# Optimization experiments

Measured on AMD Instinct MI355X. Metric: run time of the kernel, lower is better.

The kernel has to match this reference:

```python
import jax, jax.numpy as jnp
import numpy as np

B, S, T = 32, 50, 50
V_SRC, V_TRG = 32000, 32000
E, H, A = 128, 128, 128


def setup_inputs() -> dict:
    key = jax.random.key(0)
    ks = jax.random.split(key, 24)
    g = lambda k, shape, s=0.08: jax.random.normal(k, shape, dtype=jnp.float32) * s
    inp = {
        'src': jax.random.randint(ks[0], (B, S), 0, V_SRC, dtype=jnp.int32),
        'trg': jax.random.randint(ks[1], (B, T), 0, V_TRG, dtype=jnp.int32),
        'emb_src': g(ks[2], (V_SRC, E)),
        'emb_trg': g(ks[3], (V_TRG, E)),
        # PyTorch LSTM params: gates ordered (i, f, g, o)
        'enc_Wih': g(ks[4], (4 * H, E)), 'enc_Whh': g(ks[5], (4 * H, H)),
        'enc_bih': g(ks[6], (4 * H,)), 'enc_bhh': g(ks[7], (4 * H,)),
        'dec_Wih': g(ks[8], (4 * H, E)), 'dec_Whh': g(ks[9], (4 * H, H)),
        'dec_bih': g(ks[10], (4 * H,)), 'dec_bhh': g(ks[11], (4 * H,)),
        'att_w1s': g(ks[12], (A, H)), 'att_b1s': g(ks[13], (A,)),
        'att_w1t': g(ks[14], (A, H)), 'att_b1t': g(ks[15], (A,)),
        'att_w2': g(ks[16], (1, A)), 'att_b2': g(ks[17], (1,)),
        'out_w': g(ks[18], (H, 2 * H)), 'out_b': g(ks[19], (H,)),
        'sm_w': g(ks[20], (V_TRG, H)), 'sm_b': g(ks[21], (V_TRG,)),
    }
    return inp


def _lstm_cell(x, h, c, Wih, Whh, bih, bhh):
    gates = x @ Wih.T + bih + h @ Whh.T + bhh  # [B, 4H]
    i, f, g, o = jnp.split(gates, 4, axis=-1)
    c_new = jax.nn.sigmoid(f) * c + jax.nn.sigmoid(i) * jnp.tanh(g)
    h_new = jax.nn.sigmoid(o) * jnp.tanh(c_new)
    return h_new, c_new


def reference(src, trg, emb_src, emb_trg,
              enc_Wih, enc_Whh, enc_bih, enc_bhh,
              dec_Wih, dec_Whh, dec_bih, dec_bhh,
              att_w1s, att_b1s, att_w1t, att_b1t, att_w2, att_b2,
              out_w, out_b, sm_w, sm_b):
    batch = src.shape[0]
    hidden = enc_Whh.shape[1]
    h0 = jnp.zeros((batch, hidden), dtype=emb_src.dtype)
    c0 = jnp.zeros((batch, hidden), dtype=emb_src.dtype)

    # ---- encoder LSTM over src ----
    x_src = emb_src[src]                      # [B,S,E]
    def enc_step(carry, x_t):
        h, c = carry
        h, c = _lstm_cell(x_t, h, c, enc_Wih, enc_Whh, enc_bih, enc_bhh)
        return (h, c), h
    _, enc_out = jax.lax.scan(enc_step, (h0, c0), x_src.transpose(1, 0, 2))
    enc_out = enc_out.transpose(1, 0, 2)      # [B,S,H]

    # att_w1_src(src_vectors) is constant across decode steps
    att_src = enc_out @ att_w1s.T + att_b1s   # [B,S,A]

    # ---- decoder (init_hidden = zeros, per original forward) ----
    x_trg = emb_trg[trg[:, :-1]]              # [B,T-1,E]
    def dec_step(carry, x_t):
        h, c = carry
        h, c = _lstm_cell(x_t, h, c, dec_Wih, dec_Whh, dec_bih, dec_bhh)
        att_tgt = h @ att_w1t.T + att_b1t                       # [B,A]
        comb = jnp.tanh(att_src + att_tgt[:, None, :])          # [B,S,A]
        scores = (comb @ att_w2.T + att_b2)[..., 0]             # [B,S]
        align = jax.nn.softmax(scores, axis=1)
        att_vec = jnp.einsum('bs,bsh->bh', align, enc_out)      # [B,H]
        final = jnp.tanh(jnp.concatenate([h, att_vec], axis=1) @ out_w.T + out_b)
        logits = final @ sm_w.T + sm_b                          # [B,V]
        return (h, c), logits
    _, logits = jax.lax.scan(dec_step, (h0, c0), x_trg.transpose(1, 0, 2))
    return logits.transpose(1, 0, 2)          # [B,T-1,V]
```

## Files before the change

kernel.cpp:

```cpp
#include <hip/hip_runtime.h>

typedef unsigned short ushort_t;

__device__ __forceinline__ float sigf(float x) { return 1.0f / (1.0f + __expf(-x)); }
__device__ __forceinline__ float tanhf_fast(float x) { return 1.0f - 2.0f / (__expf(2.0f * x) + 1.0f); }
__device__ __forceinline__ ushort_t f2bf(float f) {
    unsigned u = __float_as_uint(f);
    unsigned r = (u + 0x7fffu + ((u >> 16) & 1u)) >> 16;
    return (ushort_t)r;
}

__global__ void transpose_kernel(const float* __restrict__ in, float* __restrict__ out,
                                 int R, int C)
{
    __shared__ float tile[32][33];
    int c0 = blockIdx.x * 32, r0 = blockIdx.y * 32;
    int x = threadIdx.x, y = threadIdx.y;
#pragma unroll
    for (int i = 0; i < 32; i += 8) {
        int r = r0 + y + i, c = c0 + x;
        if (r < R && c < C) tile[y + i][x] = in[r * C + c];
    }
    __syncthreads();
#pragma unroll
    for (int i = 0; i < 32; i += 8) {
        int r = r0 + x, c = c0 + y + i;
        if (r < R && c < C) out[c * R + r] = tile[x][y + i];
    }
}

__global__ void tok_gemv_kernel(const float* __restrict__ X,
                                const int* __restrict__ toks,
                                int divv,
                                const float* __restrict__ WT,
                                const float* __restrict__ b1,
                                const float* __restrict__ b2,
                                float* __restrict__ out,
                                int ntok)
{
    __shared__ __align__(16) float xs[4 * 128];
    int J = blockDim.x;
    int n0 = blockIdx.x * 4;
    for (int i = threadIdx.x; i < 4 * 128; i += J) {
        int tt = i >> 7, k = i & 127;
        int n = n0 + tt;
        if (n >= ntok) n = ntok - 1;
        int row;
        if (!toks) row = n;
        else if (divv == 0) row = toks[n];
        else { int bb = n / divv; int t = n - bb * divv; row = toks[bb * (divv + 1) + t]; }
        xs[i] = X[row * 128 + k];
    }
    __syncthreads();
    int j = threadIdx.x;
    float bias = b1[j] + (b2 ? b2[j] : 0.0f);
    const float4* x0 = (const float4*)(xs);
    const float4* x1 = (const float4*)(xs + 128);
    const float4* x2 = (const float4*)(xs + 256);
    const float4* x3 = (const float4*)(xs + 384);
    float a0 = 0.f, a1 = 0.f, a2 = 0.f, a3 = 0.f;
#pragma unroll 8
    for (int k4 = 0; k4 < 32; ++k4) {
        float4 v0 = x0[k4], v1 = x1[k4], v2 = x2[k4], v3 = x3[k4];
        float w0 = WT[(k4 * 4 + 0) * J + j];
        float w1 = WT[(k4 * 4 + 1) * J + j];
        float w2_ = WT[(k4 * 4 + 2) * J + j];
        float w3 = WT[(k4 * 4 + 3) * J + j];
        a0 += v0.x * w0 + v0.y * w1 + v0.z * w2_ + v0.w * w3;
        a1 += v1.x * w0 + v1.y * w1 + v1.z * w2_ + v1.w * w3;
        a2 += v2.x * w0 + v2.y * w1 + v2.z * w2_ + v2.w * w3;
        a3 += v3.x * w0 + v3.y * w1 + v3.z * w2_ + v3.w * w3;
    }
    float accs[4] = {a0, a1, a2, a3};
#pragma unroll
    for (int tt = 0; tt < 4; ++tt) {
        int n = n0 + tt;
        if (n < ntok) out[n * J + j] = bias + accs[tt];
    }
}

__global__ void __launch_bounds__(512, 2) rnn_kernel(const float* __restrict__ gih_enc,
                                                     const float* __restrict__ enc_Whh,
                                                     const float* __restrict__ gih_dec,
                                                     const float* __restrict__ dec_Whh,
                                                     float* __restrict__ enc_out,
                                                     float* __restrict__ hdec)
{
    bool is_enc = blockIdx.x < 32;
    int b = is_enc ? blockIdx.x : blockIdx.x - 32;
    int T = is_enc ? 50 : 49;
    const float* gih = is_enc ? gih_enc : gih_dec;
    const float* Whh = is_enc ? enc_Whh : dec_Whh;
    float* hout = is_enc ? enc_out : hdec;

    int tid = threadIdx.x;
    __shared__ __align__(16) float h[128];
    __shared__ float gates[512];

    float4 w[32];
    const float4* wr = (const float4*)(Whh + tid * 128);
#pragma unroll
    for (int k = 0; k < 32; ++k) w[k] = wr[k];

    float c = 0.f;
    if (tid < 128) h[tid] = 0.f;
    const float* gb = gih + b * T * 512 + tid;
    float gnext = gb[0];
    const float4* h4 = (const float4*)h;

    for (int t = 0; t < T; ++t) {
        __syncthreads();
        float acc = gnext;
        if (t + 1 < T) gnext = gb[(t + 1) * 512];
#pragma unroll
        for (int k = 0; k < 32; ++k) {
            float4 hv = h4[k];
            acc += hv.x * w[k].x + hv.y * w[k].y + hv.z * w[k].z + hv.w * w[k].w;
        }
        gates[tid] = acc;
        __syncthreads();
        if (tid < 128) {
            float gi = gates[tid], gf = gates[128 + tid], gg = gates[256 + tid], go = gates[384 + tid];
            c = sigf(gf) * c + sigf(gi) * tanhf_fast(gg);
            float hn = sigf(go) * tanhf_fast(c);
            h[tid] = hn;
            hout[(b * T + t) * 128 + tid] = hn;
        }
    }
}

__global__ void __launch_bounds__(128) att_par_kernel(const float* __restrict__ hdec,
                                                      const float* __restrict__ att_src,
                                                      const float* __restrict__ enc_out,
                                                      const float* __restrict__ w1tT,
                                                      const float* __restrict__ b1t,
                                                      const float* __restrict__ w2,
                                                      const float* __restrict__ b2,
                                                      const float* __restrict__ out_wT,
                                                      const float* __restrict__ out_b,
                                                      ushort_t* __restrict__ fin_bf)
{
    int t = blockIdx.x, b = blockIdx.y;
    int tid = threadIdx.x, lane = tid & 63, wv = tid >> 6;
    __shared__ __align__(16) float h[128];
    __shared__ __align__(16) float attv[128];
    __shared__ float attt[128];
    __shared__ float sc[64];

    h[tid] = hdec[(b * 49 + t) * 128 + tid];
    __syncthreads();
    const float4* h4 = (const float4*)h;

    {
        float acc = b1t[tid];
#pragma unroll
        for (int k4 = 0; k4 < 32; ++k4) {
            float4 hv = h4[k4];
            int k = k4 * 4;
            acc += hv.x * w1tT[(k + 0) * 128 + tid] + hv.y * w1tT[(k + 1) * 128 + tid]
                 + hv.z * w1tT[(k + 2) * 128 + tid] + hv.w * w1tT[(k + 3) * 128 + tid];
        }
        attt[tid] = acc;
    }
    __syncthreads();
    {
        float w2a = w2[lane], w2b = w2[lane + 64], b2s = b2[0];
        float ta = attt[lane], tb = attt[lane + 64];
        const float* asb = att_src + b * 6400;
        for (int s = wv; s < 50; s += 2) {
            float v = w2a * tanhf_fast(asb[s * 128 + lane] + ta)
                    + w2b * tanhf_fast(asb[s * 128 + 64 + lane] + tb);
#pragma unroll
            for (int off = 32; off; off >>= 1) v += __shfl_down(v, off);
            if (lane == 0) sc[s] = v + b2s;
        }
    }
    __syncthreads();
    if (tid < 64) {
        float x = (tid < 50) ? sc[tid] : -1e30f;
        float m = x;
#pragma unroll
        for (int off = 32; off; off >>= 1) m = fmaxf(m, __shfl_xor(m, off));
        float e = (tid < 50) ? __expf(x - m) : 0.f;
        float ssum = e;
#pragma unroll
        for (int off = 32; off; off >>= 1) ssum += __shfl_xor(ssum, off);
        if (tid < 50) sc[tid] = e / ssum;
    }
    __syncthreads();
    {
        const float* eob = enc_out + b * 6400;
        float av = 0.f;
        for (int s = 0; s < 50; ++s) av += sc[s] * eob[s * 128 + tid];
        attv[tid] = av;
    }
    __syncthreads();
    {
        const float4* av4 = (const float4*)attv;
        float a3 = out_b[tid];
#pragma unroll
        for (int k4 = 0; k4 < 32; ++k4) {
            float4 hv = h4[k4];
            int k = k4 * 4;
            a3 += hv.x * out_wT[(k + 0) * 128 + tid] + hv.y * out_wT[(k + 1) * 128 + tid]
                + hv.z * out_wT[(k + 2) * 128 + tid] + hv.w * out_wT[(k + 3) * 128 + tid];
        }
#pragma unroll
        for (int k4 = 0; k4 < 32; ++k4) {
            float4 vv = av4[k4];
            int k = 128 + k4 * 4;
            a3 += vv.x * out_wT[(k + 0) * 128 + tid] + vv.y * out_wT[(k + 1) * 128 + tid]
                + vv.z * out_wT[(k + 2) * 128 + tid] + vv.w * out_wT[(k + 3) * 128 + tid];
        }
        fin_bf[(b * 49 + t) * 128 + tid] = f2bf(tanhf_fast(a3));
    }
}

__global__ void cast_bf16_kernel(const float* __restrict__ x, ushort_t* __restrict__ y, int n)
{
    int i = (blockIdx.x * blockDim.x + threadIdx.x) * 4;
    if (i + 3 < n) {
        float4 v = *(const float4*)(x + i);
        y[i + 0] = f2bf(v.x);
        y[i + 1] = f2bf(v.y);
        y[i + 2] = f2bf(v.z);
        y[i + 3] = f2bf(v.w);
    }
}

typedef __attribute__((ext_vector_type(8))) short bfrag;
typedef __attribute__((ext_vector_type(4))) float f32x4;

__global__ void __launch_bounds__(256) logits_gemm_kernel(const ushort_t* __restrict__ A,
                                                          const ushort_t* __restrict__ Bw,
                                                          const float* __restrict__ bias,
                                                          float* __restrict__ out)
{
    int wv = threadIdx.x >> 6, lane = threadIdx.x & 63;
    int mt = blockIdx.y * 4 + wv;
    if (mt >= 98) return;
    int nbase = blockIdx.x * 128;
    int r = lane & 15;
    int kq = (lane >> 4) * 8;

    const ushort_t* ap = A + (mt * 16 + r) * 128 + kq;
    bfrag a0 = *(const bfrag*)(ap);
    bfrag a1 = *(const bfrag*)(ap + 32);
    bfrag a2 = *(const bfrag*)(ap + 64);
    bfrag a3 = *(const bfrag*)(ap + 96);

#pragma unroll
    for (int vt = 0; vt < 8; ++vt) {
        const ushort_t* bp = Bw + (nbase + vt * 16 + r) * 128 + kq;
        bfrag b0 = *(const bfrag*)(bp);
        bfrag b1 = *(const bfrag*)(bp + 32);
        bfrag b2 = *(const bfrag*)(bp + 64);
        bfrag b3 = *(const bfrag*)(bp + 96);
        f32x4 acc = {0.f, 0.f, 0.f, 0.f};
        acc = __builtin_amdgcn_mfma_f32_16x16x32_bf16(a0, b0, acc, 0, 0, 0);
        acc = __builtin_amdgcn_mfma_f32_16x16x32_bf16(a1, b1, acc, 0, 0, 0);
        acc = __builtin_amdgcn_mfma_f32_16x16x32_bf16(a2, b2, acc, 0, 0, 0);
        acc = __builtin_amdgcn_mfma_f32_16x16x32_bf16(a3, b3, acc, 0, 0, 0);
        int col = nbase + vt * 16 + r;
        float bs = bias[col];
        int mrow0 = mt * 16 + (lane >> 4) * 4;
#pragma unroll
        for (int i = 0; i < 4; ++i) out[(mrow0 + i) * 32000 + col] = acc[i] + bs;
    }
}

extern "C" void kernel_launch(void* const* d_in, const int* in_sizes, int n_in,
                              void* d_out, int out_size, void* d_ws, size_t ws_size,
                              hipStream_t stream)
{
    const int* src      = (const int*)d_in[0];
    const int* trg      = (const int*)d_in[1];
    const float* emb_src = (const float*)d_in[2];
    const float* emb_trg = (const float*)d_in[3];
    const float* enc_Wih = (const float*)d_in[4];
    const float* enc_Whh = (const float*)d_in[5];
    const float* enc_bih = (const float*)d_in[6];
    const float* enc_bhh = (const float*)d_in[7];
    const float* dec_Wih = (const float*)d_in[8];
    const float* dec_Whh = (const float*)d_in[9];
    const float* dec_bih = (const float*)d_in[10];
    const float* dec_bhh = (const float*)d_in[11];
    const float* att_w1s = (const float*)d_in[12];
    const float* att_b1s = (const float*)d_in[13];
    const float* att_w1t = (const float*)d_in[14];
    const float* att_b1t = (const float*)d_in[15];
    const float* att_w2  = (const float*)d_in[16];
    const float* att_b2  = (const float*)d_in[17];
    const float* out_w   = (const float*)d_in[18];
    const float* out_b   = (const float*)d_in[19];
    const float* sm_w    = (const float*)d_in[20];
    const float* sm_b    = (const float*)d_in[21];
    float* out = (float*)d_out;

    char* ws = (char*)d_ws;
    float*    gih_enc = (float*)(ws);
    float*    att_src = (float*)(ws);
    float*    gih_dec = (float*)(ws + 3276800);
    ushort_t* fin_bf  = (ushort_t*)(ws + 3276800);
    float*    enc_out = (float*)(ws + 6488064);
    float*    hdec    = (float*)(ws + 7307264);
    ushort_t* smw_bf  = (ushort_t*)(ws + 8110080);
    float*    WihT_e  = (float*)(ws + 16302080);
    float*    WihT_d  = (float*)(ws + 16564224);
    float*    w1sT    = (float*)(ws + 16826368);
    float*    w1tT    = (float*)(ws + 16891904);
    float*    outwT   = (float*)(ws + 16957440);

    dim3 tb(32, 8);
    transpose_kernel<<<dim3(4, 16), tb, 0, stream>>>(enc_Wih, WihT_e, 512, 128);
    transpose_kernel<<<dim3(4, 16), tb, 0, stream>>>(dec_Wih, WihT_d, 512, 128);
    transpose_kernel<<<dim3(4, 4),  tb, 0, stream>>>(att_w1s, w1sT, 128, 128);
    transpose_kernel<<<dim3(4, 4),  tb, 0, stream>>>(att_w1t, w1tT, 128, 128);
    transpose_kernel<<<dim3(8, 4),  tb, 0, stream>>>(out_w, outwT, 128, 256);

    tok_gemv_kernel<<<400, 512, 0, stream>>>(emb_src, src, 0, WihT_e, enc_bih, enc_bhh, gih_enc, 1600);
    tok_gemv_kernel<<<392, 512, 0, stream>>>(emb_trg, trg, 49, WihT_d, dec_bih, dec_bhh, gih_dec, 1568);
    cast_bf16_kernel<<<4000, 256, 0, stream>>>(sm_w, smw_bf, 32000 * 128);

    rnn_kernel<<<64, 512, 0, stream>>>(gih_enc, enc_Whh, gih_dec, dec_Whh, enc_out, hdec);

    tok_gemv_kernel<<<400, 128, 0, stream>>>(enc_out, nullptr, 0, w1sT, att_b1s, nullptr, att_src, 1600);

    att_par_kernel<<<dim3(49, 32), 128, 0, stream>>>(hdec, att_src, enc_out,
                                                     w1tT, att_b1t, att_w2, att_b2,
                                                     outwT, out_b, fin_bf);

    logits_gemm_kernel<<<dim3(250, 25), 256, 0, stream>>>(fin_bf, smw_bf, sm_b, out);
}
```

Baseline: 499.6 us.

## Merge prep kernels, fuse token GEMVs, retile logits GEMM, use packed FMA in RNN

Folds the five weight transposes and the bf16 cast of the softmax weights into one prep launch, and runs the encoder and decoder input-gate GEMVs in a single launch, cutting launch overhead. The logits GEMM now gives each wave a 64x32 tile with A fragments reused across four M tiles. Its output is written as float4 along the vocab dimension by swapping the MFMA operands. The RNN recurrence switches to float2 packed multiply-adds with two accumulators, which may change register pressure.

```diff
diff --git a/kernel.cpp b/kernel.cpp
--- a/kernel.cpp
+++ b/kernel.cpp
@@ -1,6 +1,9 @@
 #include <hip/hip_runtime.h>
 
 typedef unsigned short ushort_t;
+typedef __attribute__((ext_vector_type(2))) float f32x2;
+typedef __attribute__((ext_vector_type(8))) short bfrag;
+typedef __attribute__((ext_vector_type(4))) float f32x4;
 
 __device__ __forceinline__ float sigf(float x) { return 1.0f / (1.0f + __expf(-x)); }
 __device__ __forceinline__ float tanhf_fast(float x) { return 1.0f - 2.0f / (__expf(2.0f * x) + 1.0f); }
@@ -10,37 +13,53 @@
     return (ushort_t)r;
 }
 
-__global__ void transpose_kernel(const float* __restrict__ in, float* __restrict__ out,
-                                 int R, int C)
-{
+__global__ void prep_kernel(const float* __restrict__ eW, float* __restrict__ eWT,
+                            const float* __restrict__ dW, float* __restrict__ dWT,
+                            const float* __restrict__ w1s, float* __restrict__ w1sT,
+                            const float* __restrict__ w1t, float* __restrict__ w1tT,
+                            const float* __restrict__ ow, float* __restrict__ owT,
+                            const float* __restrict__ smw, ushort_t* __restrict__ smwbf)
+{
+    int bid = blockIdx.x;
+    int tid = threadIdx.x;
+    if (bid >= 192) {
+        int i = ((bid - 192) * 256 + tid) * 4;
+        float4 v = *(const float4*)(smw + i);
+        smwbf[i + 0] = f2bf(v.x);
+        smwbf[i + 1] = f2bf(v.y);
+        smwbf[i + 2] = f2bf(v.z);
+        smwbf[i + 3] = f2bf(v.w);
+        return;
+    }
     __shared__ float tile[32][33];
-    int c0 = blockIdx.x * 32, r0 = blockIdx.y * 32;
-    int x = threadIdx.x, y = threadIdx.y;
-#pragma unroll
-    for (int i = 0; i < 32; i += 8) {
-        int r = r0 + y + i, c = c0 + x;
-        if (r < R && c < C) tile[y + i][x] = in[r * C + c];
-    }
-    __syncthreads();
-#pragma unroll
-    for (int i = 0; i < 32; i += 8) {
-        int r = r0 + x, c = c0 + y + i;
-        if (r < R && c < C) out[c * R + r] = tile[x][y + i];
-    }
-}
-
-__global__ void tok_gemv_kernel(const float* __restrict__ X,
-                                const int* __restrict__ toks,
-                                int divv,
-                                const float* __restrict__ WT,
-                                const float* __restrict__ b1,
-                                const float* __restrict__ b2,
-                                float* __restrict__ out,
-                                int ntok)
-{
-    __shared__ __align__(16) float xs[4 * 128];
-    int J = blockDim.x;
-    int n0 = blockIdx.x * 4;
+    const float* in; float* outp; int C; int t;
+    if (bid < 64)       { in = eW;  outp = eWT;  C = 128; t = bid; }
+    else if (bid < 128) { in = dW;  outp = dWT;  C = 128; t = bid - 64; }
+    else if (bid < 144) { in = w1s; outp = w1sT; C = 128; t = bid - 128; }
+    else if (bid < 160) { in = w1t; outp = w1tT; C = 128; t = bid - 144; }
+    else                { in = ow;  outp = owT;  C = 256; t = bid - 160; }
+    int R = (bid < 128) ? 512 : 128;
+    int gx = C >> 5;
+    int c0 = (t & (gx - 1)) * 32, r0 = (t / gx) * 32;
+    int x = tid & 31, y = tid >> 5;
+#pragma unroll
+    for (int i = 0; i < 32; i += 8)
+        tile[y + i][x] = in[(r0 + y + i) * C + c0 + x];
+    __syncthreads();
+#pragma unroll
+    for (int i = 0; i < 32; i += 8)
+        outp[(c0 + y + i) * R + r0 + x] = tile[x][y + i];
+}
+
+__device__ __forceinline__ void tok_gemv_body(const float* __restrict__ X,
+                                              const int* __restrict__ toks,
+                                              int divv,
+                                              const float* __restrict__ WT,
+                                              const float* __restrict__ b1,
+                                              const float* __restrict__ b2,
+                                              float* __restrict__ out,
+                                              int ntok, int n0, int J, float* xs)
+{
     for (int i = threadIdx.x; i < 4 * 128; i += J) {
         int tt = i >> 7, k = i & 127;
         int n = n0 + tt;
@@ -79,6 +98,33 @@
     }
 }
 
+__global__ void tok_gemv_kernel(const float* __restrict__ X,
+                                const int* __restrict__ toks, int divv,
+                                const float* __restrict__ WT,
+                                const float* __restrict__ b1,
+                                const float* __restrict__ b2,
+                                float* __restrict__ out, int ntok)
+{
+    __shared__ __align__(16) float xs[4 * 128];
+    tok_gemv_body(X, toks, divv, WT, b1, b2, out, ntok, blockIdx.x * 4, blockDim.x, xs);
+}
+
+__global__ void tok_gemv2_kernel(const float* __restrict__ embS, const int* __restrict__ src,
+                                 const float* __restrict__ WTe,
+                                 const float* __restrict__ bihE, const float* __restrict__ bhhE,
+                                 float* __restrict__ gihE,
+                                 const float* __restrict__ embT, const int* __restrict__ trg,
+                                 const float* __restrict__ WTd,
+                                 const float* __restrict__ bihD, const float* __restrict__ bhhD,
+                                 float* __restrict__ gihD)
+{
+    __shared__ __align__(16) float xs[4 * 128];
+    if (blockIdx.x < 400)
+        tok_gemv_body(embS, src, 0, WTe, bihE, bhhE, gihE, 1600, blockIdx.x * 4, blockDim.x, xs);
+    else
+        tok_gemv_body(embT, trg, 49, WTd, bihD, bhhD, gihD, 1568, (blockIdx.x - 400) * 4, blockDim.x, xs);
+}
+
 __global__ void __launch_bounds__(512, 2) rnn_kernel(const float* __restrict__ gih_enc,
                                                      const float* __restrict__ enc_Whh,
                                                      const float* __restrict__ gih_dec,
@@ -97,27 +143,28 @@
     __shared__ __align__(16) float h[128];
     __shared__ float gates[512];
 
-    float4 w[32];
-    const float4* wr = (const float4*)(Whh + tid * 128);
-#pragma unroll
-    for (int k = 0; k < 32; ++k) w[k] = wr[k];
+    f32x2 w2[64];
+    const f32x2* wr = (const f32x2*)(Whh + tid * 128);
+#pragma unroll
+    for (int k = 0; k < 64; ++k) w2[k] = wr[k];
 
     float c = 0.f;
     if (tid < 128) h[tid] = 0.f;
     const float* gb = gih + b * T * 512 + tid;
     float gnext = gb[0];
-    const float4* h4 = (const float4*)h;
+    const f32x2* h2 = (const f32x2*)h;
 
     for (int t = 0; t < T; ++t) {
         __syncthreads();
-        float acc = gnext;
+        float g0 = gnext;
         if (t + 1 < T) gnext = gb[(t + 1) * 512];
-#pragma unroll
-        for (int k = 0; k < 32; ++k) {
-            float4 hv = h4[k];
-            acc += hv.x * w[k].x + hv.y * w[k].y + hv.z * w[k].z + hv.w * w[k].w;
-        }
-        gates[tid] = acc;
+        f32x2 s0 = {0.f, 0.f}, s1 = {0.f, 0.f};
+#pragma unroll
+        for (int k = 0; k < 64; k += 2) {
+            s0 += h2[k] * w2[k];
+            s1 += h2[k + 1] * w2[k + 1];
+        }
+        gates[tid] = g0 + s0.x + s0.y + s1.x + s1.y;
         __syncthreads();
         if (tid < 128) {
             float gi = gates[tid], gf = gates[128 + tid], gg = gates[256 + tid], go = gates[384 + tid];
@@ -216,56 +263,49 @@
     }
 }
 
-__global__ void cast_bf16_kernel(const float* __restrict__ x, ushort_t* __restrict__ y, int n)
-{
-    int i = (blockIdx.x * blockDim.x + threadIdx.x) * 4;
-    if (i + 3 < n) {
-        float4 v = *(const float4*)(x + i);
-        y[i + 0] = f2bf(v.x);
-        y[i + 1] = f2bf(v.y);
-        y[i + 2] = f2bf(v.z);
-        y[i + 3] = f2bf(v.w);
-    }
-}
-
-typedef __attribute__((ext_vector_type(8))) short bfrag;
-typedef __attribute__((ext_vector_type(4))) float f32x4;
-
 __global__ void __launch_bounds__(256) logits_gemm_kernel(const ushort_t* __restrict__ A,
                                                           const ushort_t* __restrict__ Bw,
                                                           const float* __restrict__ bias,
                                                           float* __restrict__ out)
 {
     int wv = threadIdx.x >> 6, lane = threadIdx.x & 63;
-    int mt = blockIdx.y * 4 + wv;
-    if (mt >= 98) return;
-    int nbase = blockIdx.x * 128;
-    int r = lane & 15;
-    int kq = (lane >> 4) * 8;
-
-    const ushort_t* ap = A + (mt * 16 + r) * 128 + kq;
-    bfrag a0 = *(const bfrag*)(ap);
-    bfrag a1 = *(const bfrag*)(ap + 32);
-    bfrag a2 = *(const bfrag*)(ap + 64);
-    bfrag a3 = *(const bfrag*)(ap + 96);
-
-#pragma unroll
-    for (int vt = 0; vt < 8; ++vt) {
-        const ushort_t* bp = Bw + (nbase + vt * 16 + r) * 128 + kq;
-        bfrag b0 = *(const bfrag*)(bp);
-        bfrag b1 = *(const bfrag*)(bp + 32);
-        bfrag b2 = *(const bfrag*)(bp + 64);
-        bfrag b3 = *(const bfrag*)(bp + 96);
-        f32x4 acc = {0.f, 0.f, 0.f, 0.f};
-        acc = __builtin_amdgcn_mfma_f32_16x16x32_bf16(a0, b0, acc, 0, 0, 0);
-        acc = __builtin_amdgcn_mfma_f32_16x16x32_bf16(a1, b1, acc, 0, 0, 0);
-        acc = __builtin_amdgcn_mfma_f32_16x16x32_bf16(a2, b2, acc, 0, 0, 0);
-        acc = __builtin_amdgcn_mfma_f32_16x16x32_bf16(a3, b3, acc, 0, 0, 0);
-        int col = nbase + vt * 16 + r;
-        float bs = bias[col];
-        int mrow0 = mt * 16 + (lane >> 4) * 4;
-#pragma unroll
-        for (int i = 0; i < 4; ++i) out[(mrow0 + i) * 32000 + col] = acc[i] + bs;
+    int r = lane & 15, kq = (lane >> 4) * 8;
+    int mbase = blockIdx.y * 64;
+    int nb = blockIdx.x * 128 + wv * 32;
+
+    bfrag a[4][4];
+#pragma unroll
+    for (int mt = 0; mt < 4; ++mt) {
+        const ushort_t* ap = A + (mbase + mt * 16 + r) * 128 + kq;
+#pragma unroll
+        for (int kk = 0; kk < 4; ++kk) a[mt][kk] = *(const bfrag*)(ap + kk * 32);
+    }
+    bfrag bf[2][4];
+#pragma unroll
+    for (int vt = 0; vt < 2; ++vt) {
+        const ushort_t* bp = Bw + (nb + vt * 16 + r) * 128 + kq;
+#pragma unroll
+        for (int kk = 0; kk < 4; ++kk) bf[vt][kk] = *(const bfrag*)(bp + kk * 32);
+    }
+
+#pragma unroll
+    for (int mt = 0; mt < 4; ++mt) {
+        bool valid = (mbase + mt * 16) < 1568;
+#pragma unroll
+        for (int vt = 0; vt < 2; ++vt) {
+            f32x4 acc = {0.f, 0.f, 0.f, 0.f};
+            acc = __builtin_amdgcn_mfma_f32_16x16x32_bf16(bf[vt][0], a[mt][0], acc, 0, 0, 0);
+            acc = __builtin_amdgcn_mfma_f32_16x16x32_bf16(bf[vt][1], a[mt][1], acc, 0, 0, 0);
+            acc = __builtin_amdgcn_mfma_f32_16x16x32_bf16(bf[vt][2], a[mt][2], acc, 0, 0, 0);
+            acc = __builtin_amdgcn_mfma_f32_16x16x32_bf16(bf[vt][3], a[mt][3], acc, 0, 0, 0);
+            if (valid) {
+                int m = mbase + mt * 16 + r;
+                int col = nb + vt * 16 + (lane >> 4) * 4;
+                float4 bs = *(const float4*)(bias + col);
+                float4 st = {acc[0] + bs.x, acc[1] + bs.y, acc[2] + bs.z, acc[3] + bs.w};
+                *(float4*)(out + (size_t)m * 32000 + col) = st;
+            }
+        }
     }
 }
 
@@ -311,16 +351,12 @@
     float*    w1tT    = (float*)(ws + 16891904);
     float*    outwT   = (float*)(ws + 16957440);
 
-    dim3 tb(32, 8);
-    transpose_kernel<<<dim3(4, 16), tb, 0, stream>>>(enc_Wih, WihT_e, 512, 128);
-    transpose_kernel<<<dim3(4, 16), tb, 0, stream>>>(dec_Wih, WihT_d, 512, 128);
-    transpose_kernel<<<dim3(4, 4),  tb, 0, stream>>>(att_w1s, w1sT, 128, 128);
-    transpose_kernel<<<dim3(4, 4),  tb, 0, stream>>>(att_w1t, w1tT, 128, 128);
-    transpose_kernel<<<dim3(8, 4),  tb, 0, stream>>>(out_w, outwT, 128, 256);
-
-    tok_gemv_kernel<<<400, 512, 0, stream>>>(emb_src, src, 0, WihT_e, enc_bih, enc_bhh, gih_enc, 1600);
-    tok_gemv_kernel<<<392, 512, 0, stream>>>(emb_trg, trg, 49, WihT_d, dec_bih, dec_bhh, gih_dec, 1568);
-    cast_bf16_kernel<<<4000, 256, 0, stream>>>(sm_w, smw_bf, 32000 * 128);
+    prep_kernel<<<4192, 256, 0, stream>>>(enc_Wih, WihT_e, dec_Wih, WihT_d,
+                                          att_w1s, w1sT, att_w1t, w1tT,
+                                          out_w, outwT, sm_w, smw_bf);
+
+    tok_gemv2_kernel<<<792, 512, 0, stream>>>(emb_src, src, WihT_e, enc_bih, enc_bhh, gih_enc,
+                                              emb_trg, trg, WihT_d, dec_bih, dec_bhh, gih_dec);
 
     rnn_kernel<<<64, 512, 0, stream>>>(gih_enc, enc_Whh, gih_dec, dec_Whh, enc_out, hdec);
 
```

After: 457.9 us. -8.4%, faster.
